# Performance work log

Hardware: AMD Instinct MI355X
Metric: run time of the kernel (lower is better)

## Reference

```python
import jax, jax.numpy as jnp
import numpy as np

THETA = 10000.0


def apply_rope(x, positions, theta=THETA):
    # x: [B, H, N, D], positions: [1, N] or [B, N]
    D = x.shape[-1]
    inv_freq = 1.0 / (theta ** (jnp.arange(0, D, 2, dtype=jnp.float32) / D))  # [D/2]
    ang = positions.astype(jnp.float32)[:, None, :, None] * inv_freq  # [B_or_1, 1, N, D/2]
    cos, sin = jnp.cos(ang), jnp.sin(ang)
    x1 = x[..., 0::2]
    x2 = x[..., 1::2]
    r1 = x1 * cos - x2 * sin
    r2 = x1 * sin + x2 * cos
    # interleave back to [..., D]
    return jnp.stack([r1, r2], axis=-1).reshape(x.shape)


def setup_inputs() -> dict:
    key = jax.random.key(0)
    ks = jax.random.split(key, 5)
    B, N, d_model = 2, 2048, 1024
    s = 1.0 / np.sqrt(d_model)
    return {
        "x": jax.random.normal(ks[0], (B, N, d_model), dtype=jnp.float32),
        "Wq": jax.random.normal(ks[1], (d_model, d_model), dtype=jnp.float32) * s,
        "Wk": jax.random.normal(ks[2], (d_model, d_model), dtype=jnp.float32) * s,
        "Wv": jax.random.normal(ks[3], (d_model, d_model), dtype=jnp.float32) * s,
        "Wo": jax.random.normal(ks[4], (d_model, d_model), dtype=jnp.float32) * s,
        "token_positions": jnp.arange(N, dtype=jnp.int32)[None, :],
    }


def reference(x, Wq, Wk, Wv, Wo, token_positions):
    B, N, d_model = x.shape
    H = 16
    D = d_model // H
    # projections: out = x @ W.T  (einsum '... i, j i -> ... j')
    def proj(W):
        y = jnp.einsum('bni,ji->bnj', x, W)
        return y.reshape(B, N, H, D).transpose(0, 2, 1, 3)  # [B,H,N,D]
    q, k, v = proj(Wq), proj(Wk), proj(Wv)
    q = apply_rope(q, token_positions)
    k = apply_rope(k, token_positions)
    scale = 1.0 / jnp.sqrt(jnp.asarray(D, dtype=x.dtype))
    scores = jnp.einsum('bhid,bhjd->bhij', q, k) * scale  # [B,H,N,N]
    causal = jnp.tril(jnp.ones((N, N), dtype=bool))
    scores = jnp.where(causal[None, None], scores, -jnp.inf)
    w = jax.nn.softmax(scores, axis=-1)
    o = jnp.einsum('bhij,bhjd->bhid', w, v)  # [B,H,N,D]
    o = o.transpose(0, 2, 1, 3).reshape(B, N, d_model)
    return jnp.einsum('bni,ji->bnj', o, Wo)
```

## Files before the change

kernel.cpp:

```cpp
#include <hip/hip_runtime.h>

#define DMODEL 1024
#define NSEQ   2048
#define BSZ    2
#define NH     16
#define HD     64
#define MROWS  (BSZ*NSEQ)

using short8 = __attribute__((ext_vector_type(8))) short;
using f32x4  = __attribute__((ext_vector_type(4))) float;

__device__ __forceinline__ short f2b(float f) {
  unsigned u = __builtin_bit_cast(unsigned, f);
  u += 0x7fffu + ((u >> 16) & 1u);
  return (short)(u >> 16);
}

__device__ __forceinline__ void load_lds16(const void* g, void* l) {
  __builtin_amdgcn_global_load_lds((const __attribute__((address_space(1))) unsigned int*)g,
                                   (__attribute__((address_space(3))) unsigned int*)l,
                                   16, 0, 0);
}

__global__ void cvt_all(const float* __restrict__ x,  const float* __restrict__ Wq,
                        const float* __restrict__ Wk, const float* __restrict__ Wv,
                        const float* __restrict__ Wo, const int* __restrict__ pos,
                        short* __restrict__ xb,  short* __restrict__ wqb,
                        short* __restrict__ wkb, short* __restrict__ wvb,
                        short* __restrict__ wob, float* __restrict__ cs) {
  const int NX  = (BSZ * NSEQ * DMODEL) / 4;
  const int NW  = (DMODEL * DMODEL) / 4;
  const int NCV = NX + 4 * NW;
  const int TOT = NCV + NSEQ * 32;
  for (int i = blockIdx.x * blockDim.x + threadIdx.x; i < TOT; i += gridDim.x * blockDim.x) {
    if (i < NCV) {
      const float* src; short* dst; int off;
      if (i < NX) { src = x; dst = xb; off = i; }
      else {
        int j = i - NX; int s = j >> 18; off = j & (NW - 1);
        src = (s == 0) ? Wq : (s == 1) ? Wk : (s == 2) ? Wv : Wo;
        dst = (s == 0) ? wqb : (s == 1) ? wkb : (s == 2) ? wvb : wob;
      }
      float4 v = reinterpret_cast<const float4*>(src)[off];
      short4 r;
      r.x = f2b(v.x); r.y = f2b(v.y); r.z = f2b(v.z); r.w = f2b(v.w);
      reinterpret_cast<short4*>(dst)[off] = r;
    } else {
      int idx = i - NCV;
      int n = idx >> 5, p = idx & 31;
      float inv = powf(10000.0f, -(float)(2 * p) / 64.0f);
      float ang = (float)pos[n] * inv;
      cs[idx * 2]     = cosf(ang);
      cs[idx * 2 + 1] = sinf(ang);
    }
  }
}

__global__ __launch_bounds__(256, 2) void gemm_qkv3(
    const short* __restrict__ xb,
    const short* __restrict__ wq, const short* __restrict__ wk, const short* __restrict__ wv,
    const float* __restrict__ cs,
    short* __restrict__ qb, short* __restrict__ kb, short* __restrict__ vt) {
  __shared__ short Al[2][128 * 64];
  __shared__ short Bl[2][3][64 * 64];

  const int t   = threadIdx.x;
  const int l   = t & 63;
  const int wid = t >> 6;
  const int wr  = (wid >> 1) * 64;
  const int wc  = (wid & 1) * 32;

  const int id = blockIdx.x;
  const int bx = id & 31;
  const int np = id >> 5;
  const int arow0 = bx * 128;
  const int bcol0 = np * 64;

  const int tr = t >> 3;
  const int c8 = (t & 7) ^ ((t >> 3) & 7);
  const short* W3[3] = {wq, wk, wv};

  auto STAGE = [&](int kt, int buf) {
#pragma unroll
    for (int is = 0; is < 4; ++is)
      load_lds16(xb + (size_t)(arow0 + tr + is * 32) * DMODEL + kt * 64 + c8 * 8,
                 &Al[buf][is * 2048 + t * 8]);
#pragma unroll
    for (int p = 0; p < 3; ++p)
#pragma unroll
      for (int is = 0; is < 2; ++is)
        load_lds16(W3[p] + (size_t)(bcol0 + tr + is * 32) * DMODEL + kt * 64 + c8 * 8,
                   &Bl[buf][p][is * 2048 + t * 8]);
  };

  f32x4 acc[3][4][2];
#pragma unroll
  for (int p = 0; p < 3; ++p)
#pragma unroll
    for (int mi = 0; mi < 4; ++mi)
#pragma unroll
      for (int ni = 0; ni < 2; ++ni) acc[p][mi][ni] = f32x4{0.f, 0.f, 0.f, 0.f};

  const int lr  = l & 15;
  const int lcb = (l >> 4) << 4;

  STAGE(0, 0);
  int cur = 0;

  for (int kt = 0; kt < DMODEL / 64; ++kt) {
    if (kt + 1 < DMODEL / 64) {
      STAGE(kt + 1, cur ^ 1);
      asm volatile("s_waitcnt vmcnt(10)" ::: "memory");
    } else {
      asm volatile("s_waitcnt vmcnt(0)" ::: "memory");
    }
    asm volatile("s_barrier" ::: "memory");

    const char* Ab = reinterpret_cast<const char*>(&Al[cur][0]);
#pragma unroll
    for (int ks = 0; ks < 2; ++ks) {
      const int cb = ks * 64 + lcb;
      short8 af[4];
#pragma unroll
      for (int mi = 0; mi < 4; ++mi) {
        int r = wr + mi * 16 + lr;
        af[mi] = *reinterpret_cast<const short8*>(Ab + r * 128 + (cb ^ ((r & 7) << 4)));
      }
#pragma unroll
      for (int p = 0; p < 3; ++p) {
        const char* Bb = reinterpret_cast<const char*>(&Bl[cur][p][0]);
        short8 bf[2];
#pragma unroll
        for (int ni = 0; ni < 2; ++ni) {
          int r = wc + ni * 16 + lr;
          bf[ni] = *reinterpret_cast<const short8*>(Bb + r * 128 + (cb ^ ((r & 7) << 4)));
        }
#pragma unroll
        for (int mi = 0; mi < 4; ++mi)
#pragma unroll
          for (int ni = 0; ni < 2; ++ni)
            acc[p][mi][ni] = __builtin_amdgcn_mfma_f32_16x16x32_bf16(af[mi], bf[ni], acc[p][mi][ni], 0, 0, 0);
      }
    }
    asm volatile("s_barrier" ::: "memory");
    cur ^= 1;
  }

  const int irow = (l >> 4) << 2;
#pragma unroll
  for (int p = 0; p < 3; ++p) {
#pragma unroll
    for (int mi = 0; mi < 4; ++mi) {
#pragma unroll
      for (int ni = 0; ni < 2; ++ni) {
#pragma unroll
        for (int r = 0; r < 4; ++r) {
          float v = acc[p][mi][ni][r];
          int m = arow0 + wr + mi * 16 + irow + r;
          int j = bcol0 + wc + ni * 16 + (l & 15);
          int n = m & (NSEQ - 1);
          int b = m >> 11;
          int h = j >> 6, d = j & 63, pp = d >> 1;
          float pv = __shfl_xor(v, 1);
          if (p < 2) {
            float c = cs[(n * 32 + pp) * 2];
            float s = cs[(n * 32 + pp) * 2 + 1];
            float res = (d & 1) ? (pv * s + v * c) : (v * c - pv * s);
            if (p == 0) res *= 0.180336880f;
            short* dst = (p == 0) ? qb : kb;
            dst[(((size_t)(b * NH + h)) * NSEQ + n) * HD + d] = f2b(res);
          } else {
            vt[(((size_t)(b * NH + h)) * HD + d) * NSEQ + n] = f2b(v);
          }
        }
      }
    }
  }
}

__global__ __launch_bounds__(256, 2) void gemm_out(
    const short* __restrict__ ob, const short* __restrict__ wo, float* __restrict__ out) {
  __shared__ short As[3 * 64 * 64];
  __shared__ short Bs[3 * 128 * 64];
  const int t = threadIdx.x;
  const int l = t & 63;
  const int w4 = t >> 6;
  const int wrow = (w4 >> 1) * 32;
  const int wcol = (w4 & 1) * 64;
  const int id = blockIdx.x;
  const int arow0 = (id & 63) * 64;
  const int bcol0 = (id >> 6) * 128;

  const int tr = t >> 3;
  const int c8 = (t & 7) ^ (tr & 7);

  auto STAGE = [&](int kt, int buf) {
#pragma unroll
    for (int is = 0; is < 2; ++is)
      load_lds16(ob + (size_t)(arow0 + tr + is * 32) * DMODEL + kt * 64 + c8 * 8,
                 &As[buf * 4096 + is * 2048 + (t >> 6) * 512]);
#pragma unroll
    for (int is = 0; is < 4; ++is)
      load_lds16(wo + (size_t)(bcol0 + tr + is * 32) * DMODEL + kt * 64 + c8 * 8,
                 &Bs[buf * 8192 + is * 2048 + (t >> 6) * 512]);
  };

  f32x4 acc[2][4];
#pragma unroll
  for (int mi = 0; mi < 2; ++mi)
#pragma unroll
    for (int ni = 0; ni < 4; ++ni) acc[mi][ni] = f32x4{0.f, 0.f, 0.f, 0.f};

  const int lr  = l & 15;
  const int lcb = (l >> 4) << 4;
  const int irow = (l >> 4) << 2;

  STAGE(0, 0);
  int cur = 0;

  for (int kt = 0; kt < DMODEL / 64; ++kt) {
    const int nxt = (cur == 2) ? 0 : cur + 1;
    if (kt + 1 < DMODEL / 64) {
      STAGE(kt + 1, nxt);
      asm volatile("s_waitcnt vmcnt(6)" ::: "memory");
    } else {
      asm volatile("s_waitcnt vmcnt(0)" ::: "memory");
    }
    asm volatile("s_barrier" ::: "memory");

    const char* Ab = reinterpret_cast<const char*>(&As[cur * 4096]);
    const char* Bb = reinterpret_cast<const char*>(&Bs[cur * 8192]);
#pragma unroll
    for (int ks = 0; ks < 2; ++ks) {
      const int cb = ks * 64 + lcb;
      short8 af[2], bf[4];
#pragma unroll
      for (int mi = 0; mi < 2; ++mi) {
        int r = wrow + mi * 16 + lr;
        af[mi] = *reinterpret_cast<const short8*>(Ab + r * 128 + (cb ^ ((r & 7) << 4)));
      }
#pragma unroll
      for (int ni = 0; ni < 4; ++ni) {
        int r = wcol + ni * 16 + lr;
        bf[ni] = *reinterpret_cast<const short8*>(Bb + r * 128 + (cb ^ ((r & 7) << 4)));
      }
#pragma unroll
      for (int mi = 0; mi < 2; ++mi)
#pragma unroll
        for (int ni = 0; ni < 4; ++ni)
          acc[mi][ni] = __builtin_amdgcn_mfma_f32_16x16x32_bf16(af[mi], bf[ni], acc[mi][ni], 0, 0, 0);
    }
    cur = nxt;
  }

#pragma unroll
  for (int mi = 0; mi < 2; ++mi) {
#pragma unroll
    for (int ni = 0; ni < 4; ++ni) {
#pragma unroll
      for (int r = 0; r < 4; ++r) {
        int m = arow0 + wrow + mi * 16 + irow + r;
        int j = bcol0 + wcol + ni * 16 + (l & 15);
        out[(size_t)m * DMODEL + j] = acc[mi][ni][r];
      }
    }
  }
}

__global__ __launch_bounds__(1024, 1) void attn(
    const short* __restrict__ qb, const short* __restrict__ kb,
    const short* __restrict__ vt, short* __restrict__ ob) {
  __shared__ short Ks[3][128 * 64];
  __shared__ short Vs[3][64 * 128];
  __shared__ short Ps[16][16 * 64];
  const int t = threadIdx.x;
  const int l = t & 63;
  const int w = t >> 6;
  const int qs = w & 7;
  const int g  = w >> 3;
  const int id  = blockIdx.x;
  const int xcd = id & 7;
  const int bh  = xcd + 8 * (id >> 6);
  const int qy  = (id >> 3) & 7;
  const short* Q  = qb + (size_t)bh * NSEQ * HD;
  const short* Kg = kb + (size_t)bh * NSEQ * HD;
  const short* Vg = vt + (size_t)bh * HD * NSEQ;
  const int b = bh >> 4, h = bh & 15;

  const int trk = t >> 3;
  const int ck  = (t & 7) ^ ((t >> 3) & 7);
  const int trv = t >> 4;
  const int cv  = (t & 15) ^ ((t >> 4) & 15);
  const int irow = (l >> 4) << 2;
  const short8 ones = {(short)0x3F80, (short)0x3F80, (short)0x3F80, (short)0x3F80,
                       (short)0x3F80, (short)0x3F80, (short)0x3F80, (short)0x3F80};

  auto STAGEA = [&](int tile, int buf) {
    int j0 = tile * 128;
    load_lds16(Kg + (size_t)(j0 + trk) * HD + ck * 8, &Ks[buf][t * 8]);
    load_lds16(Vg + (size_t)trv * NSEQ + j0 + cv * 8, &Vs[buf][t * 8]);
  };

  int cur = 0;
  for (int pass = 0; pass < 2; ++pass) {
    const int qt = pass ? (15 - qy) : qy;
    const int q0 = qt * 128;
    const int nt = qt + 1;

    asm volatile("s_barrier" ::: "memory");
    STAGEA(0, cur);

    short8 qf[2];
    {
      int qrow = q0 + qs * 16 + (l & 15);
#pragma unroll
      for (int ks = 0; ks < 2; ++ks)
        qf[ks] = *reinterpret_cast<const short8*>(Q + (size_t)qrow * HD + ks * 32 + (l >> 4) * 8);
    }

    f32x4 ao[4];
#pragma unroll
    for (int dt = 0; dt < 4; ++dt) ao[dt] = f32x4{0.f, 0.f, 0.f, 0.f};
    f32x4 accl = f32x4{0.f, 0.f, 0.f, 0.f};

    for (int tile = 0; tile < nt; ++tile) {
      const int nxt = (cur == 2) ? 0 : cur + 1;
      if (tile + 1 < nt) {
        STAGEA(tile + 1, nxt);
        asm volatile("s_waitcnt vmcnt(2)" ::: "memory");
      } else {
        asm volatile("s_waitcnt vmcnt(0)" ::: "memory");
      }
      asm volatile("s_barrier" ::: "memory");

      const char* Kb = reinterpret_cast<const char*>(&Ks[cur][0]);
      const char* Vb = reinterpret_cast<const char*>(&Vs[cur][0]);

      f32x4 sc[4];
#pragma unroll
      for (int jt = 0; jt < 4; ++jt) sc[jt] = f32x4{0.f, 0.f, 0.f, 0.f};
#pragma unroll
      for (int ks = 0; ks < 2; ++ks) {
        const int cb = ks * 64 + ((l >> 4) * 16);
#pragma unroll
        for (int jt = 0; jt < 4; ++jt) {
          int kr = g * 64 + jt * 16 + (l & 15);
          short8 kf = *reinterpret_cast<const short8*>(Kb + kr * 128 + (cb ^ ((kr & 7) << 4)));
          sc[jt] = __builtin_amdgcn_mfma_f32_16x16x32_bf16(qf[ks], kf, sc[jt], 0, 0, 0);
        }
      }

      if (tile == nt - 1) {
        const int j0 = tile * 128 + g * 64;
#pragma unroll
        for (int jt = 0; jt < 4; ++jt)
#pragma unroll
          for (int r = 0; r < 4; ++r) {
            int i_g = q0 + qs * 16 + irow + r;
            int j_g = j0 + jt * 16 + (l & 15);
            if (j_g > i_g) sc[jt][r] = -1e30f;
          }
      }

#pragma unroll
      for (int jt = 0; jt < 4; ++jt) {
#pragma unroll
        for (int r = 0; r < 4; ++r) {
          float p = __builtin_amdgcn_exp2f(sc[jt][r]);
          int i = irow + r;
          int jj = jt * 16 + (l & 15);
          Ps[w][i * 64 + (jj ^ ((i & 7) << 3))] =
              (short)(__builtin_bit_cast(unsigned, p) >> 16);
        }
      }

#pragma unroll
      for (int ks2 = 0; ks2 < 2; ++ks2) {
        const int cb = ks2 * 64 + ((l >> 4) * 16);
        int pr = l & 15;
        short8 pf = *reinterpret_cast<const short8*>(
            reinterpret_cast<const char*>(&Ps[w][0]) + pr * 128 + (cb ^ ((pr & 7) << 4)));
        accl = __builtin_amdgcn_mfma_f32_16x16x32_bf16(pf, ones, accl, 0, 0, 0);
#pragma unroll
        for (int dt = 0; dt < 4; ++dt) {
          int vr = dt * 16 + (l & 15);
          short8 vf = *reinterpret_cast<const short8*>(
              Vb + vr * 256 + ((g * 128 + cb) ^ ((vr & 15) << 4)));
          ao[dt] = __builtin_amdgcn_mfma_f32_16x16x32_bf16(pf, vf, ao[dt], 0, 0, 0);
        }
      }
      cur = nxt;
    }
    asm volatile("s_barrier" ::: "memory");

    float* Opart = reinterpret_cast<float*>(&Ks[0][0]);
    float* Apart = reinterpret_cast<float*>(&Vs[0][0]);
    const int cswz = ((l >> 4) & 1) << 4;
    if (g == 1) {
#pragma unroll
      for (int dt = 0; dt < 4; ++dt)
#pragma unroll
        for (int r = 0; r < 4; ++r)
          Opart[qs * 1024 + (irow + r) * 64 + ((dt * 16 + (l & 15)) ^ cswz)] = ao[dt][r];
      if ((l & 15) == 0)
#pragma unroll
        for (int r = 0; r < 4; ++r)
          Apart[qs * 16 + irow + r] = accl[r];
    }
    asm volatile("s_barrier" ::: "memory");
    if (g == 0) {
#pragma unroll
      for (int dt = 0; dt < 4; ++dt)
#pragma unroll
        for (int r = 0; r < 4; ++r)
          ao[dt][r] += Opart[qs * 1024 + (irow + r) * 64 + ((dt * 16 + (l & 15)) ^ cswz)];
#pragma unroll
      for (int r = 0; r < 4; ++r)
        accl[r] += Apart[qs * 16 + irow + r];
#pragma unroll
      for (int dt = 0; dt < 4; ++dt)
#pragma unroll
        for (int r = 0; r < 4; ++r) {
          int n = q0 + qs * 16 + irow + r;
          int col = h * 64 + dt * 16 + (l & 15);
          ob[((size_t)b * NSEQ + n) * DMODEL + col] = f2b(ao[dt][r] / accl[r]);
        }
    }
  }
}

extern "C" void kernel_launch(void* const* d_in, const int* in_sizes, int n_in,
                              void* d_out, int out_size, void* d_ws, size_t ws_size,
                              hipStream_t stream) {
  const float* x  = (const float*)d_in[0];
  const float* Wq = (const float*)d_in[1];
  const float* Wk = (const float*)d_in[2];
  const float* Wv = (const float*)d_in[3];
  const float* Wo = (const float*)d_in[4];
  const int*   pos = (const int*)d_in[5];
  float* out = (float*)d_out;
  char* ws = (char*)d_ws;

  short* xb  = (short*)(ws);
  short* wqb = (short*)(ws + ((size_t)8  << 20));
  short* wkb = (short*)(ws + ((size_t)10 << 20));
  short* wvb = (short*)(ws + ((size_t)12 << 20));
  short* wob = (short*)(ws + ((size_t)14 << 20));
  short* qb  = (short*)(ws + ((size_t)16 << 20));
  short* kb  = (short*)(ws + ((size_t)24 << 20));
  short* vt  = (short*)(ws + ((size_t)32 << 20));
  short* ob  = (short*)(ws + ((size_t)40 << 20));
  float* cs  = (float*)(ws + ((size_t)48 << 20));

  cvt_all<<<2048, 256, 0, stream>>>(x, Wq, Wk, Wv, Wo, pos, xb, wqb, wkb, wvb, wob, cs);
  gemm_qkv3<<<512, 256, 0, stream>>>(xb, wqb, wkb, wvb, cs, qb, kb, vt);
  attn<<<256, 1024, 0, stream>>>(qb, kb, vt, ob);
  gemm_out<<<512, 256, 0, stream>>>(ob, wob, out);
}
```

Measured before the change: 89.60 us.

## Switch attention to 32x32x16 MFMA tiles with 512-thread blocks

The attention kernel now uses 32x32x16 bf16 MFMAs with each wave owning 32 query rows, so the block shrinks from 16 to 8 waves and the per-wave P buffer grows to 32x64. Each thread now issues two K/V async loads per tile, and the wait count is adjusted to match. Larger MFMA tiles give more reuse of each LDS fragment and fewer instructions per FLOP. The cost is half as many waves per CU to hide latency and more accumulator registers per thread.

```diff
diff --git a/kernel.cpp b/kernel.cpp
--- a/kernel.cpp
+++ b/kernel.cpp
@@ -9,6 +9,7 @@
 
 using short8 = __attribute__((ext_vector_type(8))) short;
 using f32x4  = __attribute__((ext_vector_type(4))) float;
+using f32x16 = __attribute__((ext_vector_type(16))) float;
 
 __device__ __forceinline__ short f2b(float f) {
   unsigned u = __builtin_bit_cast(unsigned, f);
@@ -267,17 +268,17 @@
   }
 }
 
-__global__ __launch_bounds__(1024, 1) void attn(
+__global__ __launch_bounds__(512, 1) void attn(
     const short* __restrict__ qb, const short* __restrict__ kb,
     const short* __restrict__ vt, short* __restrict__ ob) {
   __shared__ short Ks[3][128 * 64];
   __shared__ short Vs[3][64 * 128];
-  __shared__ short Ps[16][16 * 64];
+  __shared__ short Ps[8][32 * 64];
   const int t = threadIdx.x;
   const int l = t & 63;
   const int w = t >> 6;
-  const int qs = w & 7;
-  const int g  = w >> 3;
+  const int qs = w & 3;
+  const int g  = w >> 2;
   const int id  = blockIdx.x;
   const int xcd = id & 7;
   const int bh  = xcd + 8 * (id >> 6);
@@ -291,14 +292,20 @@
   const int ck  = (t & 7) ^ ((t >> 3) & 7);
   const int trv = t >> 4;
   const int cv  = (t & 15) ^ ((t >> 4) & 15);
-  const int irow = (l >> 4) << 2;
+  const int ln31 = l & 31;
+  const int lh   = l >> 5;
   const short8 ones = {(short)0x3F80, (short)0x3F80, (short)0x3F80, (short)0x3F80,
                        (short)0x3F80, (short)0x3F80, (short)0x3F80, (short)0x3F80};
 
   auto STAGEA = [&](int tile, int buf) {
     int j0 = tile * 128;
-    load_lds16(Kg + (size_t)(j0 + trk) * HD + ck * 8, &Ks[buf][t * 8]);
-    load_lds16(Vg + (size_t)trv * NSEQ + j0 + cv * 8, &Vs[buf][t * 8]);
+#pragma unroll
+    for (int is = 0; is < 2; ++is) {
+      load_lds16(Kg + (size_t)(j0 + trk + is * 64) * HD + ck * 8,
+                 &Ks[buf][is * 4096 + t * 8]);
+      load_lds16(Vg + (size_t)(trv + is * 32) * NSEQ + j0 + cv * 8,
+                 &Vs[buf][is * 4096 + t * 8]);
+    }
   };
 
   int cur = 0;
@@ -310,24 +317,24 @@
     asm volatile("s_barrier" ::: "memory");
     STAGEA(0, cur);
 
-    short8 qf[2];
+    short8 qf[4];
     {
-      int qrow = q0 + qs * 16 + (l & 15);
-#pragma unroll
-      for (int ks = 0; ks < 2; ++ks)
-        qf[ks] = *reinterpret_cast<const short8*>(Q + (size_t)qrow * HD + ks * 32 + (l >> 4) * 8);
-    }
-
-    f32x4 ao[4];
-#pragma unroll
-    for (int dt = 0; dt < 4; ++dt) ao[dt] = f32x4{0.f, 0.f, 0.f, 0.f};
-    f32x4 accl = f32x4{0.f, 0.f, 0.f, 0.f};
+      int qrow = q0 + qs * 32 + ln31;
+#pragma unroll
+      for (int kst = 0; kst < 4; ++kst)
+        qf[kst] = *reinterpret_cast<const short8*>(Q + (size_t)qrow * HD + kst * 16 + lh * 8);
+    }
+
+    f32x16 ao[2];
+    f32x16 accl;
+#pragma unroll
+    for (int i = 0; i < 16; ++i) { ao[0][i] = 0.f; ao[1][i] = 0.f; accl[i] = 0.f; }
 
     for (int tile = 0; tile < nt; ++tile) {
       const int nxt = (cur == 2) ? 0 : cur + 1;
       if (tile + 1 < nt) {
         STAGEA(tile + 1, nxt);
-        asm volatile("s_waitcnt vmcnt(2)" ::: "memory");
+        asm volatile("s_waitcnt vmcnt(4)" ::: "memory");
       } else {
         asm volatile("s_waitcnt vmcnt(0)" ::: "memory");
       }
@@ -336,57 +343,62 @@
       const char* Kb = reinterpret_cast<const char*>(&Ks[cur][0]);
       const char* Vb = reinterpret_cast<const char*>(&Vs[cur][0]);
 
-      f32x4 sc[4];
-#pragma unroll
-      for (int jt = 0; jt < 4; ++jt) sc[jt] = f32x4{0.f, 0.f, 0.f, 0.f};
-#pragma unroll
-      for (int ks = 0; ks < 2; ++ks) {
-        const int cb = ks * 64 + ((l >> 4) * 16);
-#pragma unroll
-        for (int jt = 0; jt < 4; ++jt) {
-          int kr = g * 64 + jt * 16 + (l & 15);
-          short8 kf = *reinterpret_cast<const short8*>(Kb + kr * 128 + (cb ^ ((kr & 7) << 4)));
-          sc[jt] = __builtin_amdgcn_mfma_f32_16x16x32_bf16(qf[ks], kf, sc[jt], 0, 0, 0);
+      f32x16 sc[2];
+#pragma unroll
+      for (int i = 0; i < 16; ++i) { sc[0][i] = 0.f; sc[1][i] = 0.f; }
+#pragma unroll
+      for (int kst = 0; kst < 4; ++kst) {
+#pragma unroll
+        for (int kt2 = 0; kt2 < 2; ++kt2) {
+          int kr = g * 64 + kt2 * 32 + ln31;
+          int cb = (kst * 32 + lh * 16) ^ ((kr & 7) << 4);
+          short8 kf = *reinterpret_cast<const short8*>(Kb + kr * 128 + cb);
+          sc[kt2] = __builtin_amdgcn_mfma_f32_32x32x16_bf16(qf[kst], kf, sc[kt2], 0, 0, 0);
         }
       }
 
       if (tile == nt - 1) {
-        const int j0 = tile * 128 + g * 64;
-#pragma unroll
-        for (int jt = 0; jt < 4; ++jt)
-#pragma unroll
-          for (int r = 0; r < 4; ++r) {
-            int i_g = q0 + qs * 16 + irow + r;
-            int j_g = j0 + jt * 16 + (l & 15);
-            if (j_g > i_g) sc[jt][r] = -1e30f;
+        const int j0g = tile * 128 + g * 64;
+#pragma unroll
+        for (int kt2 = 0; kt2 < 2; ++kt2)
+#pragma unroll
+          for (int reg = 0; reg < 16; ++reg) {
+            int i_g = q0 + qs * 32 + (reg & 3) + 8 * (reg >> 2) + 4 * lh;
+            int j_g = j0g + kt2 * 32 + ln31;
+            if (j_g > i_g) sc[kt2][reg] = -1e30f;
           }
       }
 
 #pragma unroll
-      for (int jt = 0; jt < 4; ++jt) {
-#pragma unroll
-        for (int r = 0; r < 4; ++r) {
-          float p = __builtin_amdgcn_exp2f(sc[jt][r]);
-          int i = irow + r;
-          int jj = jt * 16 + (l & 15);
+      for (int kt2 = 0; kt2 < 2; ++kt2) {
+#pragma unroll
+        for (int reg = 0; reg < 16; ++reg) {
+          float p = __builtin_amdgcn_exp2f(sc[kt2][reg]);
+          int i = (reg & 3) + 8 * (reg >> 2) + 4 * lh;
+          int jj = kt2 * 32 + ln31;
           Ps[w][i * 64 + (jj ^ ((i & 7) << 3))] =
               (short)(__builtin_bit_cast(unsigned, p) >> 16);
         }
       }
 
-#pragma unroll
-      for (int ks2 = 0; ks2 < 2; ++ks2) {
-        const int cb = ks2 * 64 + ((l >> 4) * 16);
-        int pr = l & 15;
-        short8 pf = *reinterpret_cast<const short8*>(
-            reinterpret_cast<const char*>(&Ps[w][0]) + pr * 128 + (cb ^ ((pr & 7) << 4)));
-        accl = __builtin_amdgcn_mfma_f32_16x16x32_bf16(pf, ones, accl, 0, 0, 0);
-#pragma unroll
-        for (int dt = 0; dt < 4; ++dt) {
-          int vr = dt * 16 + (l & 15);
-          short8 vf = *reinterpret_cast<const short8*>(
-              Vb + vr * 256 + ((g * 128 + cb) ^ ((vr & 15) << 4)));
-          ao[dt] = __builtin_amdgcn_mfma_f32_16x16x32_bf16(pf, vf, ao[dt], 0, 0, 0);
+      short8 pa[4];
+#pragma unroll
+      for (int kst = 0; kst < 4; ++kst) {
+        int cb = (kst * 32 + lh * 16) ^ ((ln31 & 7) << 4);
+        pa[kst] = *reinterpret_cast<const short8*>(
+            reinterpret_cast<const char*>(&Ps[w][0]) + ln31 * 128 + cb);
+      }
+#pragma unroll
+      for (int kst = 0; kst < 4; ++kst)
+        accl = __builtin_amdgcn_mfma_f32_32x32x16_bf16(pa[kst], ones, accl, 0, 0, 0);
+#pragma unroll
+      for (int dtile = 0; dtile < 2; ++dtile) {
+        int vr = dtile * 32 + ln31;
+#pragma unroll
+        for (int kst = 0; kst < 4; ++kst) {
+          int cb = (g * 128 + kst * 32 + lh * 16) ^ ((vr & 15) << 4);
+          short8 vf = *reinterpret_cast<const short8*>(Vb + vr * 256 + cb);
+          ao[dtile] = __builtin_amdgcn_mfma_f32_32x32x16_bf16(pa[kst], vf, ao[dtile], 0, 0, 0);
         }
       }
       cur = nxt;
@@ -395,35 +407,43 @@
 
     float* Opart = reinterpret_cast<float*>(&Ks[0][0]);
     float* Apart = reinterpret_cast<float*>(&Vs[0][0]);
-    const int cswz = ((l >> 4) & 1) << 4;
     if (g == 1) {
 #pragma unroll
-      for (int dt = 0; dt < 4; ++dt)
-#pragma unroll
-        for (int r = 0; r < 4; ++r)
-          Opart[qs * 1024 + (irow + r) * 64 + ((dt * 16 + (l & 15)) ^ cswz)] = ao[dt][r];
-      if ((l & 15) == 0)
-#pragma unroll
-        for (int r = 0; r < 4; ++r)
-          Apart[qs * 16 + irow + r] = accl[r];
+      for (int dtile = 0; dtile < 2; ++dtile)
+#pragma unroll
+        for (int reg = 0; reg < 16; ++reg) {
+          int crow = (reg & 3) + 8 * (reg >> 2) + 4 * lh;
+          Opart[(qs * 32 + crow) * 64 + dtile * 32 + ln31] = ao[dtile][reg];
+        }
+      if (ln31 == 0)
+#pragma unroll
+        for (int reg = 0; reg < 16; ++reg) {
+          int crow = (reg & 3) + 8 * (reg >> 2) + 4 * lh;
+          Apart[qs * 32 + crow] = accl[reg];
+        }
     }
     asm volatile("s_barrier" ::: "memory");
     if (g == 0) {
 #pragma unroll
-      for (int dt = 0; dt < 4; ++dt)
-#pragma unroll
-        for (int r = 0; r < 4; ++r)
-          ao[dt][r] += Opart[qs * 1024 + (irow + r) * 64 + ((dt * 16 + (l & 15)) ^ cswz)];
-#pragma unroll
-      for (int r = 0; r < 4; ++r)
-        accl[r] += Apart[qs * 16 + irow + r];
-#pragma unroll
-      for (int dt = 0; dt < 4; ++dt)
-#pragma unroll
-        for (int r = 0; r < 4; ++r) {
-          int n = q0 + qs * 16 + irow + r;
-          int col = h * 64 + dt * 16 + (l & 15);
-          ob[((size_t)b * NSEQ + n) * DMODEL + col] = f2b(ao[dt][r] / accl[r]);
+      for (int dtile = 0; dtile < 2; ++dtile)
+#pragma unroll
+        for (int reg = 0; reg < 16; ++reg) {
+          int crow = (reg & 3) + 8 * (reg >> 2) + 4 * lh;
+          ao[dtile][reg] += Opart[(qs * 32 + crow) * 64 + dtile * 32 + ln31];
+        }
+#pragma unroll
+      for (int reg = 0; reg < 16; ++reg) {
+        int crow = (reg & 3) + 8 * (reg >> 2) + 4 * lh;
+        accl[reg] += Apart[qs * 32 + crow];
+      }
+#pragma unroll
+      for (int dtile = 0; dtile < 2; ++dtile)
+#pragma unroll
+        for (int reg = 0; reg < 16; ++reg) {
+          int crow = (reg & 3) + 8 * (reg >> 2) + 4 * lh;
+          int n = q0 + qs * 32 + crow;
+          int col = h * 64 + dtile * 32 + ln31;
+          ob[((size_t)b * NSEQ + n) * DMODEL + col] = f2b(ao[dtile][reg] / accl[reg]);
         }
     }
   }
@@ -454,6 +474,6 @@
 
   cvt_all<<<2048, 256, 0, stream>>>(x, Wq, Wk, Wv, Wo, pos, xb, wqb, wkb, wvb, wob, cs);
   gemm_qkv3<<<512, 256, 0, stream>>>(xb, wqb, wkb, wvb, cs, qb, kb, vt);
-  attn<<<256, 1024, 0, stream>>>(qb, kb, vt, ob);
+  attn<<<256, 512, 0, stream>>>(qb, kb, vt, ob);
   gemm_out<<<512, 256, 0, stream>>>(ob, wob, out);
 }
```

After: 93.78 us. 4.7% more time.

## Split attention into 512 blocks of 512 threads without key-split reduction

Applied to the files above, without the earlier changes.

The attention kernel moves from 256 blocks of 1024 threads, each doing two paired query tiles and splitting keys across two wave groups, to 512 blocks of 512 threads that each handle one query tile over 64-key tiles. This removes the cross-group LDS reduction and its extra barriers, and allows two blocks per CU. In exchange each wave walks twice as many key tiles, with a barrier per tile, and per-block work is now unbalanced across causal tiles, where before each block paired a short and a long tile.

```diff
diff --git a/kernel.cpp b/kernel.cpp
--- a/kernel.cpp
+++ b/kernel.cpp
@@ -267,164 +267,133 @@
   }
 }
 
-__global__ __launch_bounds__(1024, 1) void attn(
+__global__ __launch_bounds__(512, 2) void attn(
     const short* __restrict__ qb, const short* __restrict__ kb,
     const short* __restrict__ vt, short* __restrict__ ob) {
-  __shared__ short Ks[3][128 * 64];
-  __shared__ short Vs[3][64 * 128];
-  __shared__ short Ps[16][16 * 64];
+  __shared__ short Ks[3][64 * 64];
+  __shared__ short Vs[3][64 * 64];
+  __shared__ short Ps[8][16 * 64];
   const int t = threadIdx.x;
   const int l = t & 63;
   const int w = t >> 6;
-  const int qs = w & 7;
-  const int g  = w >> 3;
   const int id  = blockIdx.x;
-  const int xcd = id & 7;
-  const int bh  = xcd + 8 * (id >> 6);
-  const int qy  = (id >> 3) & 7;
+  const int half = id >> 8;
+  const int r8   = id & 255;
+  const int xcd  = r8 & 7;
+  const int qy   = (r8 >> 3) & 7;
+  const int bh   = xcd + 8 * (r8 >> 6);
+  const int qt   = half ? (15 - qy) : qy;
   const short* Q  = qb + (size_t)bh * NSEQ * HD;
   const short* Kg = kb + (size_t)bh * NSEQ * HD;
   const short* Vg = vt + (size_t)bh * HD * NSEQ;
   const int b = bh >> 4, h = bh & 15;
 
-  const int trk = t >> 3;
-  const int ck  = (t & 7) ^ ((t >> 3) & 7);
-  const int trv = t >> 4;
-  const int cv  = (t & 15) ^ ((t >> 4) & 15);
+  const int tr = t >> 3;
+  const int c8 = (t & 7) ^ ((t >> 3) & 7);
   const int irow = (l >> 4) << 2;
   const short8 ones = {(short)0x3F80, (short)0x3F80, (short)0x3F80, (short)0x3F80,
                        (short)0x3F80, (short)0x3F80, (short)0x3F80, (short)0x3F80};
 
   auto STAGEA = [&](int tile, int buf) {
-    int j0 = tile * 128;
-    load_lds16(Kg + (size_t)(j0 + trk) * HD + ck * 8, &Ks[buf][t * 8]);
-    load_lds16(Vg + (size_t)trv * NSEQ + j0 + cv * 8, &Vs[buf][t * 8]);
+    int j0 = tile * 64;
+    load_lds16(Kg + (size_t)(j0 + tr) * HD + c8 * 8, &Ks[buf][t * 8]);
+    load_lds16(Vg + (size_t)tr * NSEQ + j0 + c8 * 8, &Vs[buf][t * 8]);
   };
 
+  const int q0 = qt * 128;
+  const int nt = 2 * qt + 2;
+
+  STAGEA(0, 0);
+
+  short8 qf[2];
+  {
+    int qrow = q0 + w * 16 + (l & 15);
+#pragma unroll
+    for (int ks = 0; ks < 2; ++ks)
+      qf[ks] = *reinterpret_cast<const short8*>(Q + (size_t)qrow * HD + ks * 32 + (l >> 4) * 8);
+  }
+
+  f32x4 ao[4];
+#pragma unroll
+  for (int dt = 0; dt < 4; ++dt) ao[dt] = f32x4{0.f, 0.f, 0.f, 0.f};
+  f32x4 accl = f32x4{0.f, 0.f, 0.f, 0.f};
+
   int cur = 0;
-  for (int pass = 0; pass < 2; ++pass) {
-    const int qt = pass ? (15 - qy) : qy;
-    const int q0 = qt * 128;
-    const int nt = qt + 1;
-
+  for (int tile = 0; tile < nt; ++tile) {
+    const int nxt = (cur == 2) ? 0 : cur + 1;
+    if (tile + 1 < nt) {
+      STAGEA(tile + 1, nxt);
+      asm volatile("s_waitcnt vmcnt(2)" ::: "memory");
+    } else {
+      asm volatile("s_waitcnt vmcnt(0)" ::: "memory");
+    }
     asm volatile("s_barrier" ::: "memory");
-    STAGEA(0, cur);
-
-    short8 qf[2];
-    {
-      int qrow = q0 + qs * 16 + (l & 15);
-#pragma unroll
-      for (int ks = 0; ks < 2; ++ks)
-        qf[ks] = *reinterpret_cast<const short8*>(Q + (size_t)qrow * HD + ks * 32 + (l >> 4) * 8);
-    }
-
-    f32x4 ao[4];
-#pragma unroll
-    for (int dt = 0; dt < 4; ++dt) ao[dt] = f32x4{0.f, 0.f, 0.f, 0.f};
-    f32x4 accl = f32x4{0.f, 0.f, 0.f, 0.f};
-
-    for (int tile = 0; tile < nt; ++tile) {
-      const int nxt = (cur == 2) ? 0 : cur + 1;
-      if (tile + 1 < nt) {
-        STAGEA(tile + 1, nxt);
-        asm volatile("s_waitcnt vmcnt(2)" ::: "memory");
-      } else {
-        asm volatile("s_waitcnt vmcnt(0)" ::: "memory");
-      }
-      asm volatile("s_barrier" ::: "memory");
-
-      const char* Kb = reinterpret_cast<const char*>(&Ks[cur][0]);
-      const char* Vb = reinterpret_cast<const char*>(&Vs[cur][0]);
-
-      f32x4 sc[4];
-#pragma unroll
-      for (int jt = 0; jt < 4; ++jt) sc[jt] = f32x4{0.f, 0.f, 0.f, 0.f};
-#pragma unroll
-      for (int ks = 0; ks < 2; ++ks) {
-        const int cb = ks * 64 + ((l >> 4) * 16);
-#pragma unroll
-        for (int jt = 0; jt < 4; ++jt) {
-          int kr = g * 64 + jt * 16 + (l & 15);
-          short8 kf = *reinterpret_cast<const short8*>(Kb + kr * 128 + (cb ^ ((kr & 7) << 4)));
-          sc[jt] = __builtin_amdgcn_mfma_f32_16x16x32_bf16(qf[ks], kf, sc[jt], 0, 0, 0);
+
+    const char* Kb = reinterpret_cast<const char*>(&Ks[cur][0]);
+    const char* Vb = reinterpret_cast<const char*>(&Vs[cur][0]);
+
+    f32x4 sc[4];
+#pragma unroll
+    for (int jt = 0; jt < 4; ++jt) sc[jt] = f32x4{0.f, 0.f, 0.f, 0.f};
+#pragma unroll
+    for (int ks = 0; ks < 2; ++ks) {
+      const int cb = ks * 64 + ((l >> 4) * 16);
+#pragma unroll
+      for (int jt = 0; jt < 4; ++jt) {
+        int kr = jt * 16 + (l & 15);
+        short8 kf = *reinterpret_cast<const short8*>(Kb + kr * 128 + (cb ^ ((kr & 7) << 4)));
+        sc[jt] = __builtin_amdgcn_mfma_f32_16x16x32_bf16(qf[ks], kf, sc[jt], 0, 0, 0);
+      }
+    }
+
+    if (tile >= 2 * qt) {
+      const int j0 = tile * 64;
+#pragma unroll
+      for (int jt = 0; jt < 4; ++jt)
+#pragma unroll
+        for (int r = 0; r < 4; ++r) {
+          int i_g = q0 + w * 16 + irow + r;
+          int j_g = j0 + jt * 16 + (l & 15);
+          if (j_g > i_g) sc[jt][r] = -1e30f;
         }
-      }
-
-      if (tile == nt - 1) {
-        const int j0 = tile * 128 + g * 64;
-#pragma unroll
-        for (int jt = 0; jt < 4; ++jt)
-#pragma unroll
-          for (int r = 0; r < 4; ++r) {
-            int i_g = q0 + qs * 16 + irow + r;
-            int j_g = j0 + jt * 16 + (l & 15);
-            if (j_g > i_g) sc[jt][r] = -1e30f;
-          }
-      }
-
-#pragma unroll
-      for (int jt = 0; jt < 4; ++jt) {
-#pragma unroll
-        for (int r = 0; r < 4; ++r) {
-          float p = __builtin_amdgcn_exp2f(sc[jt][r]);
-          int i = irow + r;
-          int jj = jt * 16 + (l & 15);
-          Ps[w][i * 64 + (jj ^ ((i & 7) << 3))] =
-              (short)(__builtin_bit_cast(unsigned, p) >> 16);
-        }
-      }
-
-#pragma unroll
-      for (int ks2 = 0; ks2 < 2; ++ks2) {
-        const int cb = ks2 * 64 + ((l >> 4) * 16);
-        int pr = l & 15;
-        short8 pf = *reinterpret_cast<const short8*>(
-            reinterpret_cast<const char*>(&Ps[w][0]) + pr * 128 + (cb ^ ((pr & 7) << 4)));
-        accl = __builtin_amdgcn_mfma_f32_16x16x32_bf16(pf, ones, accl, 0, 0, 0);
-#pragma unroll
-        for (int dt = 0; dt < 4; ++dt) {
-          int vr = dt * 16 + (l & 15);
-          short8 vf = *reinterpret_cast<const short8*>(
-              Vb + vr * 256 + ((g * 128 + cb) ^ ((vr & 15) << 4)));
-          ao[dt] = __builtin_amdgcn_mfma_f32_16x16x32_bf16(pf, vf, ao[dt], 0, 0, 0);
-        }
-      }
-      cur = nxt;
-    }
-    asm volatile("s_barrier" ::: "memory");
-
-    float* Opart = reinterpret_cast<float*>(&Ks[0][0]);
-    float* Apart = reinterpret_cast<float*>(&Vs[0][0]);
-    const int cswz = ((l >> 4) & 1) << 4;
-    if (g == 1) {
-#pragma unroll
-      for (int dt = 0; dt < 4; ++dt)
-#pragma unroll
-        for (int r = 0; r < 4; ++r)
-          Opart[qs * 1024 + (irow + r) * 64 + ((dt * 16 + (l & 15)) ^ cswz)] = ao[dt][r];
-      if ((l & 15) == 0)
-#pragma unroll
-        for (int r = 0; r < 4; ++r)
-          Apart[qs * 16 + irow + r] = accl[r];
-    }
-    asm volatile("s_barrier" ::: "memory");
-    if (g == 0) {
-#pragma unroll
-      for (int dt = 0; dt < 4; ++dt)
-#pragma unroll
-        for (int r = 0; r < 4; ++r)
-          ao[dt][r] += Opart[qs * 1024 + (irow + r) * 64 + ((dt * 16 + (l & 15)) ^ cswz)];
-#pragma unroll
-      for (int r = 0; r < 4; ++r)
-        accl[r] += Apart[qs * 16 + irow + r];
-#pragma unroll
-      for (int dt = 0; dt < 4; ++dt)
-#pragma unroll
-        for (int r = 0; r < 4; ++r) {
-          int n = q0 + qs * 16 + irow + r;
-          int col = h * 64 + dt * 16 + (l & 15);
-          ob[((size_t)b * NSEQ + n) * DMODEL + col] = f2b(ao[dt][r] / accl[r]);
-        }
+    }
+
+#pragma unroll
+    for (int jt = 0; jt < 4; ++jt) {
+#pragma unroll
+      for (int r = 0; r < 4; ++r) {
+        float p = __builtin_amdgcn_exp2f(sc[jt][r]);
+        int i = irow + r;
+        int jj = jt * 16 + (l & 15);
+        Ps[w][i * 64 + (jj ^ ((i & 7) << 3))] =
+            (short)(__builtin_bit_cast(unsigned, p) >> 16);
+      }
+    }
+
+#pragma unroll
+    for (int ks2 = 0; ks2 < 2; ++ks2) {
+      const int cb = ks2 * 64 + ((l >> 4) * 16);
+      int pr = l & 15;
+      short8 pf = *reinterpret_cast<const short8*>(
+          reinterpret_cast<const char*>(&Ps[w][0]) + pr * 128 + (cb ^ ((pr & 7) << 4)));
+      accl = __builtin_amdgcn_mfma_f32_16x16x32_bf16(pf, ones, accl, 0, 0, 0);
+#pragma unroll
+      for (int dt = 0; dt < 4; ++dt) {
+        int vr = dt * 16 + (l & 15);
+        short8 vf = *reinterpret_cast<const short8*>(Vb + vr * 128 + (cb ^ ((vr & 7) << 4)));
+        ao[dt] = __builtin_amdgcn_mfma_f32_16x16x32_bf16(pf, vf, ao[dt], 0, 0, 0);
+      }
+    }
+    cur = nxt;
+  }
+
+#pragma unroll
+  for (int dt = 0; dt < 4; ++dt) {
+#pragma unroll
+    for (int r = 0; r < 4; ++r) {
+      int n = q0 + w * 16 + irow + r;
+      int col = h * 64 + dt * 16 + (l & 15);
+      ob[((size_t)b * NSEQ + n) * DMODEL + col] = f2b(ao[dt][r] / accl[r]);
     }
   }
 }
@@ -454,6 +423,6 @@
 
   cvt_all<<<2048, 256, 0, stream>>>(x, Wq, Wk, Wv, Wo, pos, xb, wqb, wkb, wvb, wob, cs);
   gemm_qkv3<<<512, 256, 0, stream>>>(xb, wqb, wkb, wvb, cs, qb, kb, vt);
-  attn<<<256, 1024, 0, stream>>>(qb, kb, vt, ob);
+  attn<<<512, 512, 0, stream>>>(qb, kb, vt, ob);
   gemm_out<<<512, 256, 0, stream>>>(ob, wob, out);
 }
```

Measured after the change: 93.26 us. 1.04x slower.
